# Optimization experiments

Hardware: AMD Instinct MI355X
Metric: run time of the kernel (lower is better)

Reference implementation:

```python
import jax, jax.numpy as jnp
import numpy as np

N_NODES = 100000
N_EDGES = 600000
D = 128
HEADS = 8
REL = 9
N_GRAPHS = 64


def _relconv(h, coeff, basis, w_loop, b, src, dst, etypes, n_nodes):
    # DGL RelGraphConv, basis regularizer (num_bases == num_rels), sum aggregation,
    # self-loop, bias, relu activation (dropout inactive at eval).
    W = jnp.einsum('rb,bio->rio', coeff, basis)  # [REL, D, D]
    hsrc = h[src]                                # [E, D] gather
    msg = jnp.zeros((hsrc.shape[0], W.shape[2]), h.dtype)
    for r in range(REL):  # small fixed relation set
        msg = msg + jnp.where((etypes == r)[:, None], hsrc @ W[r], 0.0)
    agg = jax.ops.segment_sum(msg, dst, num_segments=n_nodes)
    return jax.nn.relu(agg + h @ w_loop + b)


def _graph_norm(x, seg, n_graphs, w, b, ms):
    # scatter-based per-subgraph normalization (graphNorm)
    counts = jax.ops.segment_sum(jnp.ones((x.shape[0],), x.dtype), seg, num_segments=n_graphs)[:, None]
    mean = jax.ops.segment_sum(x, seg, num_segments=n_graphs) / counts
    sub = x - mean[seg] * ms
    var = jax.ops.segment_sum(sub * sub, seg, num_segments=n_graphs) / counts
    std = jnp.sqrt(var + 1e-6)
    return w * sub / std[seg] + b


def _layer_norm(x, g, b):
    mu = x.mean(-1, keepdims=True)
    v = jnp.mean((x - mu) ** 2, -1, keepdims=True)
    return g * (x - mu) / jnp.sqrt(v + 1e-5) + b


def _forward(h, src, dst, etypes, seg, num_graphs,
             q_coeff, q_basis, q_loop, q_bias,
             k_coeff, k_basis, k_loop, k_bias,
             v_coeff, v_basis, v_loop, v_bias,
             o_w, o_b, gn1_w, gn1_b, gn1_ms, ln1_g, ln1_b,
             gn2_w, gn2_b, gn2_ms, ffn1_w, ffn1_b, ffn2_w, ffn2_b,
             ln2_g, ln2_b):
    n = h.shape[0]
    hn = _graph_norm(h, seg, num_graphs, gn1_w, gn1_b, gn1_ms)
    Q = _relconv(hn, q_coeff, q_basis, q_loop, q_bias, src, dst, etypes, n)
    K = _relconv(hn, k_coeff, k_basis, k_loop, k_bias, src, dst, etypes, n)
    V = _relconv(hn, v_coeff, v_basis, v_loop, v_bias, src, dst, etypes, n)
    dh = D // HEADS
    Qh = Q.reshape(n, HEADS, dh)
    Kh = K.reshape(n, HEADS, dh)
    Vh = V.reshape(n, HEADS, dh)
    # edge dot-product attention: score_e = <K[src], Q[dst]> per head
    score = (Kh[src] * Qh[dst]).sum(-1, keepdims=True)            # [E, H, 1]
    score = jnp.exp(jnp.clip(score / np.float32(np.sqrt(dh)), -10.0, 10.0))
    wV = jax.ops.segment_sum(Vh[src] * score, dst, num_segments=n)  # [N, H, dh]
    z = jax.ops.segment_sum(score, dst, num_segments=n)             # [N, H, 1]
    attn = (wV / (z + 1e-6)).reshape(n, D)
    hO = attn @ o_w + o_b
    h1 = _layer_norm(hO, ln1_g, ln1_b)
    h2 = _graph_norm(h1, seg, num_graphs, gn2_w, gn2_b, gn2_ms)
    h3 = jax.nn.relu(h2 @ ffn1_w + ffn1_b) @ ffn2_w + ffn2_b
    return _layer_norm(h3, ln2_g, ln2_b)


def setup_inputs() -> dict:
    key = jax.random.key(0)
    ks = jax.random.split(key, 32)
    s = np.float32(1.0 / np.sqrt(D))
    inp = {
        'h': jax.random.normal(ks[0], (N_NODES, D), jnp.float32),
        'src': jax.random.randint(ks[1], (N_EDGES,), 0, N_NODES),
        'dst': jax.random.randint(ks[2], (N_EDGES,), 0, N_NODES),
        'etypes': jax.random.randint(ks[3], (N_EDGES,), 0, REL),
        'seg': jnp.sort(jax.random.randint(ks[4], (N_NODES,), 0, N_GRAPHS)),
        'num_graphs': N_GRAPHS,
    }
    def lin(k, i, o):
        return jax.random.normal(k, (i, o), jnp.float32) / np.float32(np.sqrt(i))
    for idx, nm in enumerate(['q', 'k', 'v']):
        base = 5 + idx * 4
        inp[nm + '_coeff'] = jax.random.normal(ks[base], (REL, REL), jnp.float32) / np.float32(np.sqrt(REL))
        inp[nm + '_basis'] = jax.random.normal(ks[base + 1], (REL, D, D), jnp.float32) * s
        inp[nm + '_loop'] = lin(ks[base + 2], D, D)
        inp[nm + '_bias'] = jnp.zeros((D,), jnp.float32)
    inp['o_w'] = lin(ks[17], D, D)
    inp['o_b'] = jnp.zeros((D,), jnp.float32)
    for nm in ['gn1', 'gn2']:
        inp[nm + '_w'] = jnp.ones((D,), jnp.float32)
        inp[nm + '_b'] = jnp.zeros((D,), jnp.float32)
        inp[nm + '_ms'] = jnp.ones((D,), jnp.float32)
    inp['ln1_g'] = jnp.ones((D,), jnp.float32)
    inp['ln1_b'] = jnp.zeros((D,), jnp.float32)
    inp['ln2_g'] = jnp.ones((D,), jnp.float32)
    inp['ln2_b'] = jnp.zeros((D,), jnp.float32)
    inp['ffn1_w'] = lin(ks[18], D, 2 * D)
    inp['ffn1_b'] = jnp.zeros((2 * D,), jnp.float32)
    inp['ffn2_w'] = lin(ks[19], 2 * D, D)
    inp['ffn2_b'] = jnp.zeros((D,), jnp.float32)
    return inp


def reference(h, src, dst, etypes, seg, num_graphs,
              q_coeff, q_basis, q_loop, q_bias,
              k_coeff, k_basis, k_loop, k_bias,
              v_coeff, v_basis, v_loop, v_bias,
              o_w, o_b, gn1_w, gn1_b, gn1_ms, ln1_g, ln1_b,
              gn2_w, gn2_b, gn2_ms, ffn1_w, ffn1_b, ffn2_w, ffn2_b,
              ln2_g, ln2_b):
    return _forward(h, src, dst, etypes, seg, num_graphs,
                    q_coeff, q_basis, q_loop, q_bias,
                    k_coeff, k_basis, k_loop, k_bias,
                    v_coeff, v_basis, v_loop, v_bias,
                    o_w, o_b, gn1_w, gn1_b, gn1_ms, ln1_g, ln1_b,
                    gn2_w, gn2_b, gn2_ms, ffn1_w, ffn1_b, ffn2_w, ffn2_b,
                    ln2_g, ln2_b)
```

## Files before the change

kernel.cpp:

```cpp
#include <hip/hip_runtime.h>
#include <math.h>

#define N_NODES 100000
#define N_EDGES 600000
#define D 128
#define REL 9
#define NG 64
#define NK9 (N_NODES * REL)

typedef float f32x4 __attribute__((ext_vector_type(4)));
typedef _Float16 f16x8 __attribute__((ext_vector_type(8)));
typedef _Float16 h16x2 __attribute__((ext_vector_type(2)));

__device__ __forceinline__ ushort f2h(float x) {
    union { _Float16 h; ushort u; } c; c.h = (_Float16)x; return c.u;
}
__device__ __forceinline__ float h2f(ushort u) {
    union { ushort u; _Float16 h; } c; c.u = u; return (float)c.h;
}

__device__ __forceinline__ void ld16(const ushort* g, ushort* l) {
    __builtin_amdgcn_global_load_lds(
        (const __attribute__((address_space(1))) unsigned int*)g,
        (__attribute__((address_space(3))) unsigned int*)l, 16, 0, 0);
}

__device__ __forceinline__ int lbound(const int* __restrict__ a, int n, int key) {
    int lo = 0, hi = n;
    while (lo < hi) { int mid = (lo + hi) >> 1; if (a[mid] < key) lo = mid + 1; else hi = mid; }
    return lo;
}

__global__ void hist9_kernel(const int* __restrict__ dst, const int* __restrict__ ety,
                             int* __restrict__ cnt9) {
    int e = blockIdx.x * 256 + threadIdx.x;
    if (e < N_EDGES) atomicAdd(&cnt9[dst[e] * REL + ety[e]], 1);
}

__global__ void scan1_8(const int* __restrict__ cnt, int* __restrict__ excl,
                        int* __restrict__ bsum, int n) {
    __shared__ int s[1024];
    int tid = threadIdx.x;
    int base = blockIdx.x * 8192 + tid * 8;
    int v[8]; int sum = 0;
#pragma unroll
    for (int j = 0; j < 8; ++j) { v[j] = (base + j < n) ? cnt[base + j] : 0; sum += v[j]; }
    s[tid] = sum;
    __syncthreads();
    for (int off = 1; off < 1024; off <<= 1) {
        int t = (tid >= off) ? s[tid - off] : 0;
        __syncthreads();
        s[tid] += t;
        __syncthreads();
    }
    int run = s[tid] - sum;
#pragma unroll
    for (int j = 0; j < 8; ++j) { if (base + j < n) excl[base + j] = run; run += v[j]; }
    if (tid == 1023) bsum[blockIdx.x] = s[1023];
}

__global__ void scan2_kernel(int* __restrict__ bsum, int nb) {
    __shared__ int s[128];
    int tid = threadIdx.x;
    int v = (tid < nb) ? bsum[tid] : 0;
    s[tid] = v;
    __syncthreads();
    for (int off = 1; off < 128; off <<= 1) {
        int t = (tid >= off) ? s[tid - off] : 0;
        __syncthreads();
        s[tid] += t;
        __syncthreads();
    }
    if (tid < nb) bsum[tid] = s[tid] - v;
}

__global__ void scan3_8(int* __restrict__ excl, const int* __restrict__ bsum, int n, int total) {
    int base = blockIdx.x * 8192 + threadIdx.x * 8;
    int add = bsum[blockIdx.x];
#pragma unroll
    for (int j = 0; j < 8; ++j) if (base + j < n) excl[base + j] += add;
    if (blockIdx.x == 0 && threadIdx.x == 0) excl[n] = total;
}

__global__ void scatter9_kernel(const int* __restrict__ src, const int* __restrict__ dst,
                                const int* __restrict__ ety, const int* __restrict__ rstart,
                                int* __restrict__ cur9, int* __restrict__ ssrc,
                                int* __restrict__ setp) {
    int e = blockIdx.x * 256 + threadIdx.x;
    if (e < N_EDGES) {
        int t = ety[e];
        int key = dst[e] * REL + t;
        int pos = rstart[key] + atomicAdd(&cur9[key], 1);
        ssrc[pos] = src[e];
        setp[pos] = t;
    }
}

__global__ __launch_bounds__(256)
void gn_stats(const float* __restrict__ x, const int* __restrict__ seg,
              float* __restrict__ gsum, float* __restrict__ gsumsq) {
    __shared__ float redS[8][128];
    __shared__ float redQ[8][128];
    int t = threadIdx.x;
    int c4 = (t & 31) * 4;
    int rr = t >> 5;
    int n0 = blockIdx.x * 128;
    int nend = min(n0 + 128, N_NODES);
    int len = nend - n0;
    int gfirst = seg[n0];
    int glast = seg[nend - 1];
    for (int g = gfirst; g <= glast; ++g) {
        int lo = (g == gfirst) ? n0 : n0 + lbound(seg + n0, len, g);
        int hi = (g == glast) ? nend : n0 + lbound(seg + n0, len, g + 1);
        float s0 = 0.f, s1 = 0.f, s2 = 0.f, s3 = 0.f;
        float q0 = 0.f, q1 = 0.f, q2 = 0.f, q3 = 0.f;
        for (int n = lo + rr; n < hi; n += 8) {
            float4 v = *(const float4*)&x[(size_t)n * D + c4];
            s0 += v.x; q0 += v.x * v.x;
            s1 += v.y; q1 += v.y * v.y;
            s2 += v.z; q2 += v.z * v.z;
            s3 += v.w; q3 += v.w * v.w;
        }
        redS[rr][c4 + 0] = s0; redS[rr][c4 + 1] = s1;
        redS[rr][c4 + 2] = s2; redS[rr][c4 + 3] = s3;
        redQ[rr][c4 + 0] = q0; redQ[rr][c4 + 1] = q1;
        redQ[rr][c4 + 2] = q2; redQ[rr][c4 + 3] = q3;
        __syncthreads();
        if (t < 128) {
            float ts = 0.f, tq = 0.f;
#pragma unroll
            for (int ph = 0; ph < 8; ++ph) { ts += redS[ph][t]; tq += redQ[ph][t]; }
            atomicAdd(&gsum[g * D + t], ts);
            atomicAdd(&gsumsq[g * D + t], tq);
        }
        __syncthreads();
    }
}

__global__ __launch_bounds__(256)
void gn_stats_h(const ushort* __restrict__ x, const int* __restrict__ seg,
                float* __restrict__ gsum, float* __restrict__ gsumsq) {
    __shared__ float redS[8][128];
    __shared__ float redQ[8][128];
    int t = threadIdx.x;
    int c4 = (t & 31) * 4;
    int rr = t >> 5;
    int n0 = blockIdx.x * 128;
    int nend = min(n0 + 128, N_NODES);
    int len = nend - n0;
    int gfirst = seg[n0];
    int glast = seg[nend - 1];
    for (int g = gfirst; g <= glast; ++g) {
        int lo = (g == gfirst) ? n0 : n0 + lbound(seg + n0, len, g);
        int hi = (g == glast) ? nend : n0 + lbound(seg + n0, len, g + 1);
        float s0 = 0.f, s1 = 0.f, s2 = 0.f, s3 = 0.f;
        float q0 = 0.f, q1 = 0.f, q2 = 0.f, q3 = 0.f;
        for (int n = lo + rr; n < hi; n += 8) {
            ushort4 u = *(const ushort4*)&x[(size_t)n * D + c4];
            float v0 = h2f(u.x), v1 = h2f(u.y), v2 = h2f(u.z), v3 = h2f(u.w);
            s0 += v0; q0 += v0 * v0;
            s1 += v1; q1 += v1 * v1;
            s2 += v2; q2 += v2 * v2;
            s3 += v3; q3 += v3 * v3;
        }
        redS[rr][c4 + 0] = s0; redS[rr][c4 + 1] = s1;
        redS[rr][c4 + 2] = s2; redS[rr][c4 + 3] = s3;
        redQ[rr][c4 + 0] = q0; redQ[rr][c4 + 1] = q1;
        redQ[rr][c4 + 2] = q2; redQ[rr][c4 + 3] = q3;
        __syncthreads();
        if (t < 128) {
            float ts = 0.f, tq = 0.f;
#pragma unroll
            for (int ph = 0; ph < 8; ++ph) { ts += redS[ph][t]; tq += redQ[ph][t]; }
            atomicAdd(&gsum[g * D + t], ts);
            atomicAdd(&gsumsq[g * D + t], tq);
        }
        __syncthreads();
    }
}

__global__ void gn_final(const float* __restrict__ gsum, const float* __restrict__ gsumsq,
                         const int* __restrict__ seg, const float* __restrict__ w,
                         const float* __restrict__ b, const float* __restrict__ ms,
                         float* __restrict__ sc, float* __restrict__ off) {
    int g = blockIdx.x, ch = threadIdx.x;
    int lo = lbound(seg, N_NODES, g), hi = lbound(seg, N_NODES, g + 1);
    float cnt = (float)max(hi - lo, 1);
    float mean = gsum[g * D + ch] / cnt;
    float mm = mean * ms[ch];
    float var = gsumsq[g * D + ch] / cnt - 2.f * mm * mean + mm * mm;
    float rstd = rsqrtf(var + 1e-6f);
    float s = w[ch] * rstd;
    sc[g * D + ch] = s;
    off[g * D + ch] = b[ch] - s * mm;
}

__global__ __launch_bounds__(256)
void gn_apply(const float* __restrict__ x, const int* __restrict__ seg,
              const float* __restrict__ sc, const float* __restrict__ off,
              ushort* __restrict__ outhf) {
    int t = blockIdx.x * 256 + threadIdx.x;
    int n = t >> 6;
    if (n >= N_NODES) return;
    int ch = (t & 63) * 2;
    int g = seg[n];
    float2 xv = *(const float2*)&x[(size_t)n * D + ch];
    float2 s2 = *(const float2*)&sc[g * D + ch];
    float2 o2 = *(const float2*)&off[g * D + ch];
    ushort2 o;
    o.x = f2h(s2.x * xv.x + o2.x);
    o.y = f2h(s2.y * xv.y + o2.y);
    *(ushort2*)&outhf[(size_t)n * D + ch] = o;
}

__global__ __launch_bounds__(256)
void gn_apply_h(const ushort* __restrict__ x, const int* __restrict__ seg,
                const float* __restrict__ sc, const float* __restrict__ off,
                ushort* __restrict__ outhf) {
    int t = blockIdx.x * 256 + threadIdx.x;
    int n = t >> 6;
    if (n >= N_NODES) return;
    int ch = (t & 63) * 2;
    int g = seg[n];
    ushort2 xv = *(const ushort2*)&x[(size_t)n * D + ch];
    float2 s2 = *(const float2*)&sc[g * D + ch];
    float2 o2 = *(const float2*)&off[g * D + ch];
    ushort2 o;
    o.x = f2h(s2.x * h2f(xv.x) + o2.x);
    o.y = f2h(s2.y * h2f(xv.y) + o2.y);
    *(ushort2*)&outhf[(size_t)n * D + ch] = o;
}

__global__ void build_bt_qkv3(const float* __restrict__ c0, const float* __restrict__ c1,
                              const float* __restrict__ c2, const float* __restrict__ b0,
                              const float* __restrict__ b1, const float* __restrict__ b2,
                              const float* __restrict__ l0, const float* __restrict__ l1,
                              const float* __restrict__ l2, const float* __restrict__ i0,
                              const float* __restrict__ i1, const float* __restrict__ i2,
                              ushort* __restrict__ Btqkv, float* __restrict__ biasq) {
    int pj = blockIdx.y;
    const float* coeff  = pj == 0 ? c0 : (pj == 1 ? c1 : c2);
    const float* basis  = pj == 0 ? b0 : (pj == 1 ? b1 : b2);
    const float* loop_w = pj == 0 ? l0 : (pj == 1 ? l1 : l2);
    const float* bin    = pj == 0 ? i0 : (pj == 1 ? i1 : i2);
    ushort* Bt = Btqkv + (size_t)pj * 128 * 1280;
    int t = blockIdx.x * 256 + threadIdx.x;
    if (t < 128) biasq[pj * 128 + t] = bin[t];
    if (t >= 128 * 1280) return;
    int o = t / 1280;
    int k = t - o * 1280;
    float v;
    if (k < 128) {
        v = loop_w[k * 128 + o];
    } else {
        int kk = k - 128;
        int r = kk >> 7, i = kk & 127;
        v = 0.f;
#pragma unroll
        for (int b = 0; b < REL; ++b)
            v += coeff[r * REL + b] * basis[((size_t)b * 128 + i) * 128 + o];
    }
    Bt[(size_t)o * 1280 + k] = f2h(v);
}

__global__ void transpose_cast3(const float* __restrict__ o_w, ushort* __restrict__ Bto,
                                const float* __restrict__ f1, ushort* __restrict__ Btf1,
                                const float* __restrict__ f2, ushort* __restrict__ Btf2) {
    int t = blockIdx.x * 256 + threadIdx.x;
    if (t < 16384) {
        int n = t >> 7, k = t & 127;
        Bto[(size_t)n * 128 + k] = f2h(o_w[(size_t)k * 128 + n]);
    } else if (t < 49152) {
        int u = t - 16384;
        int n = u >> 7, k = u & 127;
        Btf1[(size_t)n * 128 + k] = f2h(f1[(size_t)k * 256 + n]);
    } else if (t < 81920) {
        int u = t - 49152;
        int n = u >> 8, k = u & 255;
        Btf2[(size_t)n * 256 + k] = f2h(f2[(size_t)k * 128 + n]);
    }
}

__global__ __launch_bounds__(256)
void s_pass(const ushort* __restrict__ hnhf, const int* __restrict__ ssrc,
            const int* __restrict__ setp, const int* __restrict__ rstart,
            ushort* __restrict__ Ab, int c0, int c1) {
    int n = c0 + ((blockIdx.x * 256 + threadIdx.x) >> 6);
    if (n >= c1) return;
    int lane = threadIdx.x & 63;
    int e0 = rstart[n * REL], e1 = rstart[n * REL + REL];
    h16x2 a0 = (h16x2)0, a1 = (h16x2)0, a2 = (h16x2)0, a3 = (h16x2)0, a4 = (h16x2)0;
    h16x2 a5 = (h16x2)0, a6 = (h16x2)0, a7 = (h16x2)0, a8 = (h16x2)0;
#define ACC(rr, hv) switch (rr) { \
        case 0: a0 += hv; break; case 1: a1 += hv; break; case 2: a2 += hv; break; \
        case 3: a3 += hv; break; case 4: a4 += hv; break; case 5: a5 += hv; break; \
        case 6: a6 += hv; break; case 7: a7 += hv; break; default: a8 += hv; break; }
    int e = e0;
    for (; e + 4 <= e1; e += 4) {
        int s0 = ssrc[e], s1 = ssrc[e + 1], s2 = ssrc[e + 2], s3 = ssrc[e + 3];
        int r0 = __builtin_amdgcn_readfirstlane(setp[e]);
        int r1 = __builtin_amdgcn_readfirstlane(setp[e + 1]);
        int r2 = __builtin_amdgcn_readfirstlane(setp[e + 2]);
        int r3 = __builtin_amdgcn_readfirstlane(setp[e + 3]);
        h16x2 hv0 = *(const h16x2*)&hnhf[(size_t)s0 * D + 2 * lane];
        h16x2 hv1 = *(const h16x2*)&hnhf[(size_t)s1 * D + 2 * lane];
        h16x2 hv2 = *(const h16x2*)&hnhf[(size_t)s2 * D + 2 * lane];
        h16x2 hv3 = *(const h16x2*)&hnhf[(size_t)s3 * D + 2 * lane];
        ACC(r0, hv0)
        ACC(r1, hv1)
        ACC(r2, hv2)
        ACC(r3, hv3)
    }
    for (; e < e1; ++e) {
        int s0 = ssrc[e];
        int r0 = __builtin_amdgcn_readfirstlane(setp[e]);
        h16x2 hv0 = *(const h16x2*)&hnhf[(size_t)s0 * D + 2 * lane];
        ACC(r0, hv0)
    }
#undef ACC
    ushort* arow = Ab + (size_t)(n - c0) * 1152;
#define ST(r) *(h16x2*)&arow[r * 128 + 2 * lane] = a##r;
    ST(0) ST(1) ST(2) ST(3) ST(4) ST(5) ST(6) ST(7) ST(8)
#undef ST
}

__global__ __launch_bounds__(512)
void mfma_gemm384(const ushort* __restrict__ A1, const ushort* __restrict__ Ab, int M,
                  const ushort* __restrict__ Bt, const float* __restrict__ bias,
                  ushort* __restrict__ Cout) {
    __shared__ ushort As[128 * 64];
    __shared__ ushort Bs[384 * 64];
    const int tid = threadIdx.x;
    const int lane = tid & 63;
    const int wave = tid >> 6;
    const int wm = wave & 1, wn = wave >> 1;
    const int quad = lane >> 4, l16 = lane & 15;
    const int row0 = blockIdx.x * 128;

    const ushort* sA1[2];
    const ushort* sA2[2];
#pragma unroll
    for (int i = 0; i < 2; ++i) {
        int rs = (wave * 2 + i) * 8 + (lane >> 3);
        int kg = (lane & 7) ^ (rs & 7);
        int ra = row0 + rs; if (ra >= M) ra = M - 1;
        sA1[i] = A1 + (size_t)ra * 128 + kg * 8;
        sA2[i] = Ab + (size_t)ra * 1152 + kg * 8;
    }
    const ushort* sB[6];
#pragma unroll
    for (int i = 0; i < 6; ++i) {
        int rs = (wave * 6 + i) * 8 + (lane >> 3);
        int kg = (lane & 7) ^ (rs & 7);
        sB[i] = Bt + (size_t)rs * 1280 + kg * 8;
    }

    f32x4 acc[4][6];
#pragma unroll
    for (int i = 0; i < 4; ++i)
#pragma unroll
        for (int j = 0; j < 6; ++j) acc[i][j] = (f32x4){0.f, 0.f, 0.f, 0.f};

    for (int kc = 0; kc < 1280; kc += 64) {
#pragma unroll
        for (int i = 0; i < 6; ++i) ld16(sB[i] + kc, &Bs[(wave * 6 + i) * 512]);
#pragma unroll
        for (int i = 0; i < 2; ++i) {
            const ushort* as = (kc < 128) ? (sA1[i] + kc) : (sA2[i] + (kc - 128));
            ld16(as, &As[(wave * 2 + i) * 512]);
        }
        __syncthreads();
#pragma unroll
        for (int h = 0; h < 2; ++h) {
            f16x8 af[4], bf[6];
#pragma unroll
            for (int i = 0; i < 4; ++i) {
                int r = wm * 64 + i * 16 + l16;
                af[i] = *(const f16x8*)&As[r * 64 + (((h * 4 + quad) ^ (r & 7)) * 8)];
            }
#pragma unroll
            for (int j = 0; j < 6; ++j) {
                int c = wn * 96 + j * 16 + l16;
                bf[j] = *(const f16x8*)&Bs[c * 64 + (((h * 4 + quad) ^ (c & 7)) * 8)];
            }
#pragma unroll
            for (int i = 0; i < 4; ++i)
#pragma unroll
                for (int j = 0; j < 6; ++j)
                    acc[i][j] = __builtin_amdgcn_mfma_f32_16x16x32_f16(af[i], bf[j], acc[i][j], 0, 0, 0);
        }
        __syncthreads();
    }

#pragma unroll
    for (int i = 0; i < 4; ++i) {
        int gr0 = wm * 64 + i * 16 + quad * 4 + row0;
#pragma unroll
        for (int r = 0; r < 4; ++r) {
            int gr = gr0 + r;
            if (gr >= M) continue;
#pragma unroll
            for (int j = 0; j < 6; ++j) {
                int gcol = wn * 96 + j * 16 + l16;
                float v = acc[i][j][r] + bias[gcol];
                v = fmaxf(v, 0.f);
                Cout[(size_t)gr * 384 + gcol] = f2h(v);
            }
        }
    }
}

template<bool F16OUT>
__global__ __launch_bounds__(256, 3)
void mfma_gemm_ln(const ushort* __restrict__ A, int lda, int M,
                  const ushort* __restrict__ Bt, int K,
                  const float* __restrict__ bias, const float* __restrict__ lng,
                  const float* __restrict__ lnb, void* __restrict__ Cout) {
    __shared__ ushort As[128 * 64];
    __shared__ ushort Bs[128 * 64];
    __shared__ float rsum[2][128];
    __shared__ float rsq[2][128];
    const int tid = threadIdx.x;
    const int lane = tid & 63;
    const int wave = tid >> 6;
    const int wm = wave & 1, wn = wave >> 1;
    const int quad = lane >> 4, l16 = lane & 15;
    const int row0 = blockIdx.y * 128;

    const ushort* sA[4];
    const ushort* sB[4];
#pragma unroll
    for (int i = 0; i < 4; ++i) {
        int rs = (wave * 4 + i) * 8 + (lane >> 3);
        int kg = (lane & 7) ^ (rs & 7);
        int ra = row0 + rs; if (ra >= M) ra = M - 1;
        sA[i] = A + (size_t)ra * lda + kg * 8;
        sB[i] = Bt + (size_t)rs * K + kg * 8;
    }

    f32x4 acc[4][4];
#pragma unroll
    for (int i = 0; i < 4; ++i)
#pragma unroll
        for (int j = 0; j < 4; ++j) acc[i][j] = (f32x4){0.f, 0.f, 0.f, 0.f};

    for (int kc = 0; kc < K; kc += 64) {
#pragma unroll
        for (int i = 0; i < 4; ++i) {
            ld16(sA[i] + kc, &As[(wave * 4 + i) * 512]);
            ld16(sB[i] + kc, &Bs[(wave * 4 + i) * 512]);
        }
        __syncthreads();
#pragma unroll
        for (int h = 0; h < 2; ++h) {
            f16x8 af[4], bf[4];
#pragma unroll
            for (int i = 0; i < 4; ++i) {
                int r = wm * 64 + i * 16 + l16;
                af[i] = *(const f16x8*)&As[r * 64 + (((h * 4 + quad) ^ (r & 7)) * 8)];
                int c = wn * 64 + i * 16 + l16;
                bf[i] = *(const f16x8*)&Bs[c * 64 + (((h * 4 + quad) ^ (c & 7)) * 8)];
            }
#pragma unroll
            for (int i = 0; i < 4; ++i)
#pragma unroll
                for (int j = 0; j < 4; ++j)
                    acc[i][j] = __builtin_amdgcn_mfma_f32_16x16x32_f16(af[i], bf[j], acc[i][j], 0, 0, 0);
        }
        __syncthreads();
    }

#pragma unroll
    for (int i = 0; i < 4; ++i) {
#pragma unroll
        for (int r = 0; r < 4; ++r) {
            float s = 0.f, q = 0.f;
#pragma unroll
            for (int j = 0; j < 4; ++j) {
                float v = acc[i][j][r] + bias[wn * 64 + j * 16 + l16];
                s += v; q += v * v;
            }
            s += __shfl_xor(s, 1); q += __shfl_xor(q, 1);
            s += __shfl_xor(s, 2); q += __shfl_xor(q, 2);
            s += __shfl_xor(s, 4); q += __shfl_xor(q, 4);
            s += __shfl_xor(s, 8); q += __shfl_xor(q, 8);
            if (l16 == 0) {
                int row = wm * 64 + i * 16 + quad * 4 + r;
                rsum[wn][row] = s;
                rsq[wn][row] = q;
            }
        }
    }
    __syncthreads();

#pragma unroll
    for (int i = 0; i < 4; ++i) {
#pragma unroll
        for (int r = 0; r < 4; ++r) {
            int row = wm * 64 + i * 16 + quad * 4 + r;
            int grow = row0 + row;
            if (grow >= M) continue;
            float tot = rsum[0][row] + rsum[1][row];
            float tq  = rsq[0][row] + rsq[1][row];
            float mu = tot * (1.f / 128.f);
            float var = tq * (1.f / 128.f) - mu * mu;
            float rstd = rsqrtf(var + 1e-5f);
#pragma unroll
            for (int j = 0; j < 4; ++j) {
                int gcol = wn * 64 + j * 16 + l16;
                float v = acc[i][j][r] + bias[gcol];
                float o = lng[gcol] * (v - mu) * rstd + lnb[gcol];
                if (F16OUT) ((ushort*)Cout)[(size_t)grow * 128 + gcol] = f2h(o);
                else        ((float*)Cout)[(size_t)grow * 128 + gcol] = o;
            }
        }
    }
}

__global__ __launch_bounds__(512)
void ffn_fused(const ushort* __restrict__ A, int M,
               const ushort* __restrict__ B1t, const float* __restrict__ b1,
               const ushort* __restrict__ B2t, const float* __restrict__ b2,
               const float* __restrict__ lng, const float* __restrict__ lnb,
               float* __restrict__ Cout) {
    extern __shared__ ushort sh[];
    ushort* As   = sh;
    ushort* Bs   = sh + 128 * 64;
    ushort* C1s  = sh + 128 * 64 + 256 * 64;
    float*  rsum = (float*)(C1s + 128 * 256);
    float*  rsq  = rsum + 4 * 128;
    const int tid = threadIdx.x;
    const int lane = tid & 63;
    const int wave = tid >> 6;
    const int quad = lane >> 4, l16 = lane & 15;
    const int row0 = blockIdx.x * 128;

    {
        const int wm = wave & 1, wn = wave >> 1;
        const ushort* sA[2];
#pragma unroll
        for (int i = 0; i < 2; ++i) {
            int rs = (wave * 2 + i) * 8 + (lane >> 3);
            int kg = (lane & 7) ^ (rs & 7);
            int ra = row0 + rs; if (ra >= M) ra = M - 1;
            sA[i] = A + (size_t)ra * 128 + kg * 8;
        }
        const ushort* sB[4];
#pragma unroll
        for (int i = 0; i < 4; ++i) {
            int rs = (wave * 4 + i) * 8 + (lane >> 3);
            int kg = (lane & 7) ^ (rs & 7);
            sB[i] = B1t + (size_t)rs * 128 + kg * 8;
        }
        f32x4 acc[4][4];
#pragma unroll
        for (int i = 0; i < 4; ++i)
#pragma unroll
            for (int j = 0; j < 4; ++j) acc[i][j] = (f32x4){0.f, 0.f, 0.f, 0.f};

        for (int kc = 0; kc < 128; kc += 64) {
#pragma unroll
            for (int i = 0; i < 4; ++i) ld16(sB[i] + kc, &Bs[(wave * 4 + i) * 512]);
#pragma unroll
            for (int i = 0; i < 2; ++i) ld16(sA[i] + kc, &As[(wave * 2 + i) * 512]);
            __syncthreads();
#pragma unroll
            for (int h = 0; h < 2; ++h) {
                f16x8 af[4], bf[4];
#pragma unroll
                for (int i = 0; i < 4; ++i) {
                    int r = wm * 64 + i * 16 + l16;
                    af[i] = *(const f16x8*)&As[r * 64 + (((h * 4 + quad) ^ (r & 7)) * 8)];
                }
#pragma unroll
                for (int j = 0; j < 4; ++j) {
                    int c = wn * 64 + j * 16 + l16;
                    bf[j] = *(const f16x8*)&Bs[c * 64 + (((h * 4 + quad) ^ (c & 7)) * 8)];
                }
#pragma unroll
                for (int i = 0; i < 4; ++i)
#pragma unroll
                    for (int j = 0; j < 4; ++j)
                        acc[i][j] = __builtin_amdgcn_mfma_f32_16x16x32_f16(af[i], bf[j], acc[i][j], 0, 0, 0);
            }
            __syncthreads();
        }

#pragma unroll
        for (int i = 0; i < 4; ++i) {
            int lr0 = wm * 64 + i * 16 + quad * 4;
#pragma unroll
            for (int r = 0; r < 4; ++r) {
                int row = lr0 + r;
                int rw = row & 7;
#pragma unroll
                for (int j = 0; j < 4; ++j) {
                    int cbase = j * 16 + l16;
                    int kg = cbase >> 3;
                    float v = acc[i][j][r] + b1[wn * 64 + cbase];
                    v = fmaxf(v, 0.f);
                    C1s[row * 256 + wn * 64 + ((kg ^ rw) * 8) + (cbase & 7)] = f2h(v);
                }
            }
        }
    }
    __syncthreads();

    {
        const int wm = wave & 1, wn = wave >> 1;
        const ushort* sB[2];
#pragma unroll
        for (int i = 0; i < 2; ++i) {
            int rs = (wave * 2 + i) * 8 + (lane >> 3);
            int kg = (lane & 7) ^ (rs & 7);
            sB[i] = B2t + (size_t)rs * 256 + kg * 8;
        }
        f32x4 acc[4][2];
#pragma unroll
        for (int i = 0; i < 4; ++i)
#pragma unroll
            for (int j = 0; j < 2; ++j) acc[i][j] = (f32x4){0.f, 0.f, 0.f, 0.f};

        for (int kc = 0; kc < 256; kc += 64) {
#pragma unroll
            for (int i = 0; i < 2; ++i) ld16(sB[i] + kc, &Bs[(wave * 2 + i) * 512]);
            __syncthreads();
#pragma unroll
            for (int h = 0; h < 2; ++h) {
                f16x8 af[4], bf[2];
#pragma unroll
                for (int i = 0; i < 4; ++i) {
                    int r = wm * 64 + i * 16 + l16;
                    af[i] = *(const f16x8*)&C1s[r * 256 + kc + (((h * 4 + quad) ^ (r & 7)) * 8)];
                }
#pragma unroll
                for (int j = 0; j < 2; ++j) {
                    int c = wn * 32 + j * 16 + l16;
                    bf[j] = *(const f16x8*)&Bs[c * 64 + (((h * 4 + quad) ^ (c & 7)) * 8)];
                }
#pragma unroll
                for (int i = 0; i < 4; ++i)
#pragma unroll
                    for (int j = 0; j < 2; ++j)
                        acc[i][j] = __builtin_amdgcn_mfma_f32_16x16x32_f16(af[i], bf[j], acc[i][j], 0, 0, 0);
            }
            __syncthreads();
        }

#pragma unroll
        for (int i = 0; i < 4; ++i) {
#pragma unroll
            for (int r = 0; r < 4; ++r) {
                float s = 0.f, q = 0.f;
#pragma unroll
                for (int j = 0; j < 2; ++j) {
                    float v = acc[i][j][r] + b2[wn * 32 + j * 16 + l16];
                    s += v; q += v * v;
                }
                s += __shfl_xor(s, 1); q += __shfl_xor(q, 1);
                s += __shfl_xor(s, 2); q += __shfl_xor(q, 2);
                s += __shfl_xor(s, 4); q += __shfl_xor(q, 4);
                s += __shfl_xor(s, 8); q += __shfl_xor(q, 8);
                if (l16 == 0) {
                    int row = wm * 64 + i * 16 + quad * 4 + r;
                    rsum[wn * 128 + row] = s;
                    rsq[wn * 128 + row] = q;
                }
            }
        }
        __syncthreads();

#pragma unroll
        for (int i = 0; i < 4; ++i) {
#pragma unroll
            for (int r = 0; r < 4; ++r) {
                int row = wm * 64 + i * 16 + quad * 4 + r;
                int grow = row0 + row;
                if (grow >= M) continue;
                float tot = rsum[row] + rsum[128 + row] + rsum[256 + row] + rsum[384 + row];
                float tq  = rsq[row] + rsq[128 + row] + rsq[256 + row] + rsq[384 + row];
                float mu = tot * (1.f / 128.f);
                float var = tq * (1.f / 128.f) - mu * mu;
                float rstd = rsqrtf(var + 1e-5f);
#pragma unroll
                for (int j = 0; j < 2; ++j) {
                    int gcol = wn * 32 + j * 16 + l16;
                    float v = acc[i][j][r] + b2[gcol];
                    float o = lng[gcol] * (v - mu) * rstd + lnb[gcol];
                    Cout[(size_t)grow * 128 + gcol] = o;
                }
            }
        }
    }
}

__global__ __launch_bounds__(256)
void attn_kernel(const ushort* __restrict__ C, const int* __restrict__ ssrc,
                 const int* __restrict__ rstart, ushort* __restrict__ attnhf) {
    int n = (blockIdx.x * 256 + threadIdx.x) >> 6;
    if (n >= N_NODES) return;
    int lane = threadIdx.x & 63;
    h16x2 qh = *(const h16x2*)&C[(size_t)n * 384 + 2 * lane];
    int e0 = rstart[n * REL], e1 = rstart[n * REL + REL];
    float wvx = 0.f, wvy = 0.f, z = 0.f;
    int e = e0;
    for (; e + 8 <= e1; e += 8) {
        int s[8];
#pragma unroll
        for (int j = 0; j < 8; ++j) s[j] = ssrc[e + j];
        h16x2 kk[8], vv[8];
#pragma unroll
        for (int j = 0; j < 8; ++j) kk[j] = *(const h16x2*)&C[(size_t)s[j] * 384 + 128 + 2 * lane];
#pragma unroll
        for (int j = 0; j < 8; ++j) vv[j] = *(const h16x2*)&C[(size_t)s[j] * 384 + 256 + 2 * lane];
        float d[8];
#pragma unroll
        for (int j = 0; j < 8; ++j) d[j] = __builtin_amdgcn_fdot2(kk[j], qh, 0.f, false);
#pragma unroll
        for (int j = 0; j < 8; ++j) d[j] += __shfl_xor(d[j], 1);
#pragma unroll
        for (int j = 0; j < 8; ++j) d[j] += __shfl_xor(d[j], 2);
#pragma unroll
        for (int j = 0; j < 8; ++j) d[j] += __shfl_xor(d[j], 4);
#pragma unroll
        for (int j = 0; j < 8; ++j) {
            float sc = __expf(fminf(fmaxf(d[j] * 0.25f, -10.f), 10.f));
            wvx += sc * (float)vv[j].x;
            wvy += sc * (float)vv[j].y;
            z += sc;
        }
    }
    for (; e + 4 <= e1; e += 4) {
        int s0 = ssrc[e], s1 = ssrc[e + 1], s2 = ssrc[e + 2], s3 = ssrc[e + 3];
        h16x2 k0 = *(const h16x2*)&C[(size_t)s0 * 384 + 128 + 2 * lane];
        h16x2 k1 = *(const h16x2*)&C[(size_t)s1 * 384 + 128 + 2 * lane];
        h16x2 k2 = *(const h16x2*)&C[(size_t)s2 * 384 + 128 + 2 * lane];
        h16x2 k3 = *(const h16x2*)&C[(size_t)s3 * 384 + 128 + 2 * lane];
        h16x2 v0 = *(const h16x2*)&C[(size_t)s0 * 384 + 256 + 2 * lane];
        h16x2 v1 = *(const h16x2*)&C[(size_t)s1 * 384 + 256 + 2 * lane];
        h16x2 v2 = *(const h16x2*)&C[(size_t)s2 * 384 + 256 + 2 * lane];
        h16x2 v3 = *(const h16x2*)&C[(size_t)s3 * 384 + 256 + 2 * lane];
        float d0 = __builtin_amdgcn_fdot2(k0, qh, 0.f, false);
        float d1 = __builtin_amdgcn_fdot2(k1, qh, 0.f, false);
        float d2 = __builtin_amdgcn_fdot2(k2, qh, 0.f, false);
        float d3 = __builtin_amdgcn_fdot2(k3, qh, 0.f, false);
        d0 += __shfl_xor(d0, 1); d1 += __shfl_xor(d1, 1);
        d2 += __shfl_xor(d2, 1); d3 += __shfl_xor(d3, 1);
        d0 += __shfl_xor(d0, 2); d1 += __shfl_xor(d1, 2);
        d2 += __shfl_xor(d2, 2); d3 += __shfl_xor(d3, 2);
        d0 += __shfl_xor(d0, 4); d1 += __shfl_xor(d1, 4);
        d2 += __shfl_xor(d2, 4); d3 += __shfl_xor(d3, 4);
        float sc0 = __expf(fminf(fmaxf(d0 * 0.25f, -10.f), 10.f));
        float sc1 = __expf(fminf(fmaxf(d1 * 0.25f, -10.f), 10.f));
        float sc2 = __expf(fminf(fmaxf(d2 * 0.25f, -10.f), 10.f));
        float sc3 = __expf(fminf(fmaxf(d3 * 0.25f, -10.f), 10.f));
        wvx += sc0 * (float)v0.x + sc1 * (float)v1.x;
        wvy += sc0 * (float)v0.y + sc1 * (float)v1.y;
        wvx += sc2 * (float)v2.x + sc3 * (float)v3.x;
        wvy += sc2 * (float)v2.y + sc3 * (float)v3.y;
        z += sc0 + sc1 + sc2 + sc3;
    }
    for (; e < e1; ++e) {
        int s0 = ssrc[e];
        h16x2 k0 = *(const h16x2*)&C[(size_t)s0 * 384 + 128 + 2 * lane];
        h16x2 v0 = *(const h16x2*)&C[(size_t)s0 * 384 + 256 + 2 * lane];
        float d0 = __builtin_amdgcn_fdot2(k0, qh, 0.f, false);
        d0 += __shfl_xor(d0, 1);
        d0 += __shfl_xor(d0, 2);
        d0 += __shfl_xor(d0, 4);
        float sc0 = __expf(fminf(fmaxf(d0 * 0.25f, -10.f), 10.f));
        wvx += sc0 * (float)v0.x;
        wvy += sc0 * (float)v0.y;
        z += sc0;
    }
    float inv = 1.f / (z + 1e-6f);
    ushort2 o;
    o.x = f2h(wvx * inv);
    o.y = f2h(wvy * inv);
    *(ushort2*)&attnhf[(size_t)n * D + 2 * lane] = o;
}

extern "C" void kernel_launch(void* const* d_in, const int* in_sizes, int n_in,
                              void* d_out, int out_size, void* d_ws, size_t ws_size,
                              hipStream_t stream) {
    (void)in_sizes; (void)n_in; (void)out_size;
    const float* h     = (const float*)d_in[0];
    const int*   src   = (const int*)d_in[1];
    const int*   dst   = (const int*)d_in[2];
    const int*   ety   = (const int*)d_in[3];
    const int*   seg   = (const int*)d_in[4];
    const float* coeffs[3] = {(const float*)d_in[6],  (const float*)d_in[10], (const float*)d_in[14]};
    const float* bases [3] = {(const float*)d_in[7],  (const float*)d_in[11], (const float*)d_in[15]};
    const float* loops [3] = {(const float*)d_in[8],  (const float*)d_in[12], (const float*)d_in[16]};
    const float* pbias [3] = {(const float*)d_in[9],  (const float*)d_in[13], (const float*)d_in[17]};
    const float* o_w   = (const float*)d_in[18];
    const float* o_b   = (const float*)d_in[19];
    const float* gn1_w = (const float*)d_in[20];
    const float* gn1_b = (const float*)d_in[21];
    const float* gn1_ms= (const float*)d_in[22];
    const float* gn2_w = (const float*)d_in[23];
    const float* gn2_b = (const float*)d_in[24];
    const float* gn2_ms= (const float*)d_in[25];
    const float* ln1_g = (const float*)d_in[26];
    const float* ln1_b = (const float*)d_in[27];
    const float* ln2_g = (const float*)d_in[28];
    const float* ln2_b = (const float*)d_in[29];
    const float* ffn1_w= (const float*)d_in[30];
    const float* ffn1_b= (const float*)d_in[31];
    const float* ffn2_w= (const float*)d_in[32];
    const float* ffn2_b= (const float*)d_in[33];

    char* p = (char*)d_ws;
    auto take = [&](size_t bytes) { char* r = p; p += (bytes + 255) & ~(size_t)255; return r; };
    int*    cnt9   = (int*)take((size_t)NK9 * 2 * 4);
    int*    cur9   = cnt9 + NK9;
    int*    rstart = (int*)take((size_t)(NK9 + 8) * 4);
    int*    bsum   = (int*)take(512);
    int*    ssrc   = (int*)take((size_t)N_EDGES * 4);
    int*    setp   = (int*)take((size_t)N_EDGES * 4);
    float*  gsum   = (float*)take((size_t)NG * D * 4 * 2);
    float*  gsumsq = gsum + NG * D;
    float*  gsc    = (float*)take((size_t)NG * D * 4);
    float*  goff   = (float*)take((size_t)NG * D * 4);
    ushort* Btqkv  = (ushort*)take((size_t)384 * 1280 * 2);
    float*  biasq  = (float*)take(384 * 4);
    ushort* Bto    = (ushort*)take((size_t)128 * 128 * 2);
    ushort* Btf1   = (ushort*)take((size_t)256 * 128 * 2);
    ushort* Btf2   = (ushort*)take((size_t)128 * 256 * 2);
    ushort* hnhf   = (ushort*)take((size_t)N_NODES * D * 2);
    ushort* attnhf = (ushort*)take((size_t)N_NODES * D * 2);
    ushort* h1hf   = (ushort*)take((size_t)N_NODES * D * 2);
    ushort* Cqkv   = (ushort*)take((size_t)N_NODES * 384 * 2);
    size_t used = (size_t)(p - (char*)d_ws);
    size_t avail = (ws_size > used) ? ws_size - used : 0;
    int NC = 1;
    if (avail < (size_t)N_NODES * 1152 * 2) NC = 4;
    if (NC == 4 && avail < ((size_t)(N_NODES / 4 + 1) * 1152 * 2)) NC = 8;
    ushort* Ab = (ushort*)p;
    const int chunk = (N_NODES + NC - 1) / NC;

    ushort* gn2hf  = Cqkv;

    const int EB = (N_EDGES + 255) / 256;
    const int KB = (NK9 + 8191) / 8192;
    const int WB = (N_NODES * 64 + 255) / 256;
    const int GB = (N_NODES + 127) / 128;
    const int RB = (N_NODES + 127) / 128;

    hipMemsetAsync(cnt9, 0, (size_t)NK9 * 8, stream);
    hist9_kernel<<<EB, 256, 0, stream>>>(dst, ety, cnt9);
    scan1_8<<<KB, 1024, 0, stream>>>(cnt9, rstart, bsum, NK9);
    scan2_kernel<<<1, 128, 0, stream>>>(bsum, KB);
    scan3_8<<<KB, 1024, 0, stream>>>(rstart, bsum, NK9, N_EDGES);
    scatter9_kernel<<<EB, 256, 0, stream>>>(src, dst, ety, rstart, cur9, ssrc, setp);

    build_bt_qkv3<<<dim3(640, 3), 256, 0, stream>>>(
        coeffs[0], coeffs[1], coeffs[2], bases[0], bases[1], bases[2],
        loops[0], loops[1], loops[2], pbias[0], pbias[1], pbias[2], Btqkv, biasq);
    transpose_cast3<<<320, 256, 0, stream>>>(o_w, Bto, ffn1_w, Btf1, ffn2_w, Btf2);

    hipMemsetAsync(gsum, 0, (size_t)NG * D * 8, stream);
    gn_stats<<<GB, 256, 0, stream>>>(h, seg, gsum, gsumsq);
    gn_final<<<NG, 128, 0, stream>>>(gsum, gsumsq, seg, gn1_w, gn1_b, gn1_ms, gsc, goff);
    gn_apply<<<WB, 256, 0, stream>>>(h, seg, gsc, goff, hnhf);

    for (int c = 0; c < NC; ++c) {
        int c0 = c * chunk;
        int c1 = min(N_NODES, c0 + chunk);
        int rows = c1 - c0;
        if (rows <= 0) break;
        s_pass<<<(rows + 3) / 4, 256, 0, stream>>>(hnhf, ssrc, setp, rstart, Ab, c0, c1);
        mfma_gemm384<<<(rows + 127) / 128, 512, 0, stream>>>(
            hnhf + (size_t)c0 * 128, Ab, rows, Btqkv, biasq, Cqkv + (size_t)c0 * 384);
    }

    attn_kernel<<<WB, 256, 0, stream>>>(Cqkv, ssrc, rstart, attnhf);

    mfma_gemm_ln<true><<<dim3(1, RB), 256, 0, stream>>>(
        attnhf, 128, N_NODES, Bto, 128, o_b, ln1_g, ln1_b, h1hf);

    hipMemsetAsync(gsum, 0, (size_t)NG * D * 8, stream);
    gn_stats_h<<<GB, 256, 0, stream>>>(h1hf, seg, gsum, gsumsq);
    gn_final<<<NG, 128, 0, stream>>>(gsum, gsumsq, seg, gn2_w, gn2_b, gn2_ms, gsc, goff);
    gn_apply_h<<<WB, 256, 0, stream>>>(h1hf, seg, gsc, goff, gn2hf);

    const int FFN_LDS = (128 * 64 + 256 * 64 + 128 * 256) * 2 + 4 * 128 * 4 * 2;
    hipFuncSetAttribute((const void*)ffn_fused, hipFuncAttributeMaxDynamicSharedMemorySize, FFN_LDS);
    ffn_fused<<<RB, 512, FFN_LDS, stream>>>(
        gn2hf, N_NODES, Btf1, ffn1_b, Btf2, ffn2_b, ln2_g, ln2_b, (float*)d_out);
}
```

Baseline: 750.8 us.

## Shrink fused FFN row tile to 64 and pad intermediate LDS instead of swizzle

The fused FFN kernel now processes 64 rows per block instead of 128, halving per-wave accumulators and cutting LDS use from about 100KB to about 70KB. This doubles the block count and may allow more blocks per CU, trading some reuse of the B weight tiles for occupancy. The intermediate C1 buffer switches from XOR swizzling to a padded row stride of 264 to avoid bank conflicts with simpler addressing.

```diff
diff --git a/kernel.cpp b/kernel.cpp
--- a/kernel.cpp
+++ b/kernel.cpp
@@ -7,6 +7,7 @@
 #define REL 9
 #define NG 64
 #define NK9 (N_NODES * REL)
+#define C1LD 264
 
 typedef float f32x4 __attribute__((ext_vector_type(4)));
 typedef _Float16 f16x8 __attribute__((ext_vector_type(8)));
@@ -525,26 +526,22 @@
                float* __restrict__ Cout) {
     extern __shared__ ushort sh[];
     ushort* As   = sh;
-    ushort* Bs   = sh + 128 * 64;
-    ushort* C1s  = sh + 128 * 64 + 256 * 64;
-    float*  rsum = (float*)(C1s + 128 * 256);
-    float*  rsq  = rsum + 4 * 128;
+    ushort* Bs   = sh + 64 * 64;
+    ushort* C1s  = sh + 64 * 64 + 256 * 64;
+    float*  rsum = (float*)(C1s + 64 * C1LD);
+    float*  rsq  = rsum + 4 * 64;
     const int tid = threadIdx.x;
     const int lane = tid & 63;
     const int wave = tid >> 6;
+    const int wm = wave & 1, wn = wave >> 1;
     const int quad = lane >> 4, l16 = lane & 15;
-    const int row0 = blockIdx.x * 128;
+    const int row0 = blockIdx.x * 64;
 
     {
-        const int wm = wave & 1, wn = wave >> 1;
-        const ushort* sA[2];
-#pragma unroll
-        for (int i = 0; i < 2; ++i) {
-            int rs = (wave * 2 + i) * 8 + (lane >> 3);
-            int kg = (lane & 7) ^ (rs & 7);
-            int ra = row0 + rs; if (ra >= M) ra = M - 1;
-            sA[i] = A + (size_t)ra * 128 + kg * 8;
-        }
+        int rsA = wave * 8 + (lane >> 3);
+        int kgA = (lane & 7) ^ (rsA & 7);
+        int raA = row0 + rsA; if (raA >= M) raA = M - 1;
+        const ushort* sA = A + (size_t)raA * 128 + kgA * 8;
         const ushort* sB[4];
 #pragma unroll
         for (int i = 0; i < 4; ++i) {
@@ -552,24 +549,23 @@
             int kg = (lane & 7) ^ (rs & 7);
             sB[i] = B1t + (size_t)rs * 128 + kg * 8;
         }
-        f32x4 acc[4][4];
-#pragma unroll
-        for (int i = 0; i < 4; ++i)
+        f32x4 acc[2][4];
+#pragma unroll
+        for (int i = 0; i < 2; ++i)
 #pragma unroll
             for (int j = 0; j < 4; ++j) acc[i][j] = (f32x4){0.f, 0.f, 0.f, 0.f};
 
         for (int kc = 0; kc < 128; kc += 64) {
 #pragma unroll
             for (int i = 0; i < 4; ++i) ld16(sB[i] + kc, &Bs[(wave * 4 + i) * 512]);
-#pragma unroll
-            for (int i = 0; i < 2; ++i) ld16(sA[i] + kc, &As[(wave * 2 + i) * 512]);
+            ld16(sA + kc, &As[wave * 512]);
             __syncthreads();
 #pragma unroll
             for (int h = 0; h < 2; ++h) {
-                f16x8 af[4], bf[4];
-#pragma unroll
-                for (int i = 0; i < 4; ++i) {
-                    int r = wm * 64 + i * 16 + l16;
+                f16x8 af[2], bf[4];
+#pragma unroll
+                for (int i = 0; i < 2; ++i) {
+                    int r = wm * 32 + i * 16 + l16;
                     af[i] = *(const f16x8*)&As[r * 64 + (((h * 4 + quad) ^ (r & 7)) * 8)];
                 }
 #pragma unroll
@@ -578,7 +574,7 @@
                     bf[j] = *(const f16x8*)&Bs[c * 64 + (((h * 4 + quad) ^ (c & 7)) * 8)];
                 }
 #pragma unroll
-                for (int i = 0; i < 4; ++i)
+                for (int i = 0; i < 2; ++i)
 #pragma unroll
                     for (int j = 0; j < 4; ++j)
                         acc[i][j] = __builtin_amdgcn_mfma_f32_16x16x32_f16(af[i], bf[j], acc[i][j], 0, 0, 0);
@@ -587,19 +583,17 @@
         }
 
 #pragma unroll
-        for (int i = 0; i < 4; ++i) {
-            int lr0 = wm * 64 + i * 16 + quad * 4;
+        for (int i = 0; i < 2; ++i) {
+            int lr0 = wm * 32 + i * 16 + quad * 4;
 #pragma unroll
             for (int r = 0; r < 4; ++r) {
                 int row = lr0 + r;
-                int rw = row & 7;
 #pragma unroll
                 for (int j = 0; j < 4; ++j) {
-                    int cbase = j * 16 + l16;
-                    int kg = cbase >> 3;
-                    float v = acc[i][j][r] + b1[wn * 64 + cbase];
+                    int col = wn * 64 + j * 16 + l16;
+                    float v = acc[i][j][r] + b1[col];
                     v = fmaxf(v, 0.f);
-                    C1s[row * 256 + wn * 64 + ((kg ^ rw) * 8) + (cbase & 7)] = f2h(v);
+                    C1s[row * C1LD + col] = f2h(v);
                 }
             }
         }
@@ -607,7 +601,6 @@
     __syncthreads();
 
     {
-        const int wm = wave & 1, wn = wave >> 1;
         const ushort* sB[2];
 #pragma unroll
         for (int i = 0; i < 2; ++i) {
@@ -615,9 +608,9 @@
             int kg = (lane & 7) ^ (rs & 7);
             sB[i] = B2t + (size_t)rs * 256 + kg * 8;
         }
-        f32x4 acc[4][2];
-#pragma unroll
-        for (int i = 0; i < 4; ++i)
+        f32x4 acc[2][2];
+#pragma unroll
+        for (int i = 0; i < 2; ++i)
 #pragma unroll
             for (int j = 0; j < 2; ++j) acc[i][j] = (f32x4){0.f, 0.f, 0.f, 0.f};
 
@@ -627,11 +620,11 @@
             __syncthreads();
 #pragma unroll
             for (int h = 0; h < 2; ++h) {
-                f16x8 af[4], bf[2];
-#pragma unroll
-                for (int i = 0; i < 4; ++i) {
-                    int r = wm * 64 + i * 16 + l16;
-                    af[i] = *(const f16x8*)&C1s[r * 256 + kc + (((h * 4 + quad) ^ (r & 7)) * 8)];
+                f16x8 af[2], bf[2];
+#pragma unroll
+                for (int i = 0; i < 2; ++i) {
+                    int r = wm * 32 + i * 16 + l16;
+                    af[i] = *(const f16x8*)&C1s[r * C1LD + kc + ((h * 4 + quad) * 8)];
                 }
 #pragma unroll
                 for (int j = 0; j < 2; ++j) {
@@ -639,7 +632,7 @@
                     bf[j] = *(const f16x8*)&Bs[c * 64 + (((h * 4 + quad) ^ (c & 7)) * 8)];
                 }
 #pragma unroll
-                for (int i = 0; i < 4; ++i)
+                for (int i = 0; i < 2; ++i)
 #pragma unroll
                     for (int j = 0; j < 2; ++j)
                         acc[i][j] = __builtin_amdgcn_mfma_f32_16x16x32_f16(af[i], bf[j], acc[i][j], 0, 0, 0);
@@ -648,7 +641,7 @@
         }
 
 #pragma unroll
-        for (int i = 0; i < 4; ++i) {
+        for (int i = 0; i < 2; ++i) {
 #pragma unroll
             for (int r = 0; r < 4; ++r) {
                 float s = 0.f, q = 0.f;
@@ -662,23 +655,23 @@
                 s += __shfl_xor(s, 4); q += __shfl_xor(q, 4);
                 s += __shfl_xor(s, 8); q += __shfl_xor(q, 8);
                 if (l16 == 0) {
-                    int row = wm * 64 + i * 16 + quad * 4 + r;
-                    rsum[wn * 128 + row] = s;
-                    rsq[wn * 128 + row] = q;
+                    int row = wm * 32 + i * 16 + quad * 4 + r;
+                    rsum[wn * 64 + row] = s;
+                    rsq[wn * 64 + row] = q;
                 }
             }
         }
         __syncthreads();
 
 #pragma unroll
-        for (int i = 0; i < 4; ++i) {
+        for (int i = 0; i < 2; ++i) {
 #pragma unroll
             for (int r = 0; r < 4; ++r) {
-                int row = wm * 64 + i * 16 + quad * 4 + r;
+                int row = wm * 32 + i * 16 + quad * 4 + r;
                 int grow = row0 + row;
                 if (grow >= M) continue;
-                float tot = rsum[row] + rsum[128 + row] + rsum[256 + row] + rsum[384 + row];
-                float tq  = rsq[row] + rsq[128 + row] + rsq[256 + row] + rsq[384 + row];
+                float tot = rsum[row] + rsum[64 + row] + rsum[128 + row] + rsum[192 + row];
+                float tq  = rsq[row] + rsq[64 + row] + rsq[128 + row] + rsq[192 + row];
                 float mu = tot * (1.f / 128.f);
                 float var = tq * (1.f / 128.f) - mu * mu;
                 float rstd = rsqrtf(var + 1e-5f);
@@ -846,6 +839,7 @@
     const int WB = (N_NODES * 64 + 255) / 256;
     const int GB = (N_NODES + 127) / 128;
     const int RB = (N_NODES + 127) / 128;
+    const int FB = (N_NODES + 63) / 64;
 
     hipMemsetAsync(cnt9, 0, (size_t)NK9 * 8, stream);
     hist9_kernel<<<EB, 256, 0, stream>>>(dst, ety, cnt9);
@@ -884,8 +878,8 @@
     gn_final<<<NG, 128, 0, stream>>>(gsum, gsumsq, seg, gn2_w, gn2_b, gn2_ms, gsc, goff);
     gn_apply_h<<<WB, 256, 0, stream>>>(h1hf, seg, gsc, goff, gn2hf);
 
-    const int FFN_LDS = (128 * 64 + 256 * 64 + 128 * 256) * 2 + 4 * 128 * 4 * 2;
+    const int FFN_LDS = (64 * 64 + 256 * 64 + 64 * C1LD) * 2 + 2 * 4 * 64 * 4;
     hipFuncSetAttribute((const void*)ffn_fused, hipFuncAttributeMaxDynamicSharedMemorySize, FFN_LDS);
-    ffn_fused<<<RB, 512, FFN_LDS, stream>>>(
+    ffn_fused<<<FB, 512, FFN_LDS, stream>>>(
         gn2hf, N_NODES, Btf1, ffn1_b, Btf2, ffn2_b, ln2_g, ln2_b, (float*)d_out);
 }
```

Result: faster. 718.4 us (-4.3%).
